# Performance work log

Measured on AMD Instinct MI355X. Metric: run time of the kernel, lower is better.

The kernel has to match this reference:

```python
import jax, jax.numpy as jnp
import numpy as np

C = 32          # in_channels
K = 16          # cluster_nums
G = 16          # grid size per axis (64 / window 4)
FW = 4          # window size
H = G * FW      # 64
NG = G ** 3     # 4096 nodes
NC = NG // K    # 256 nodes per cluster (balanced)
EPS = 1e-5


def setup_inputs():
    key = jax.random.key(0)
    ks = jax.random.split(key, 10)
    def w(k, shape, s=0.05):
        return jax.random.normal(k, shape, jnp.float32) * s
    # balanced cluster assignment (each cluster has exactly NC nodes)
    rng = np.random.RandomState(0)
    ci = np.repeat(np.arange(K, dtype=np.int32), NC)
    rng.shuffle(ci)
    return {
        "x_concat": jax.random.normal(ks[0], (1, H, H, H, C), jnp.float32),
        "cluster_index": jnp.asarray(ci),
        # per-cluster Adjacent_matrix params (1x1 conv == per-pixel linear)
        "conv1_w": w(ks[1], (K, 2 * C, C)), "conv1_b": jnp.zeros((K, 2 * C)),
        "bn1_g": jnp.ones((K, 2 * C)), "bn1_b": jnp.zeros((K, 2 * C)),
        "conv2_w": w(ks[2], (K, 3 * C, 2 * C)), "conv2_b": jnp.zeros((K, 3 * C)),
        "bn2_g": jnp.ones((K, 3 * C)), "bn2_b": jnp.zeros((K, 3 * C)),
        "conv3_w": w(ks[3], (K, 3 * C)), "conv3_b": jnp.zeros((K,)),
        # per-cluster GCN params
        "gcn_w": w(ks[4], (K, 2 * C, C)),
        "bn3_g": jnp.ones((K, C)), "bn3_b": jnp.zeros((K, C)),
        # shared MLP producing spatial weight [C,C] from centroid
        "mlp_w1": w(ks[5], (C, C * C // 8)), "mlp_b1": jnp.zeros((C * C // 8,)),
        "mlp_w2": w(ks[6], (C * C // 8, C * C // 4)), "mlp_b2": jnp.zeros((C * C // 4,)),
        "mlp_w3": w(ks[7], (C * C // 4, C * C)), "mlp_b3": jnp.zeros((C * C,)),
    }


def _bn(h, g, b, axes):
    # train-mode BatchNorm (biased batch statistics), dropout treated as eval/no-op
    m = h.mean(axes, keepdims=True)
    v = h.var(axes, keepdims=True)
    return (h - m) * jax.lax.rsqrt(v + EPS) * g + b


def _forward(cluster_index, x_concat, conv1_w, conv1_b, bn1_g, bn1_b,
             conv2_w, conv2_b, bn2_g, bn2_b, conv3_w, conv3_b,
             gcn_w, bn3_g, bn3_b,
             mlp_w1, mlp_b1, mlp_w2, mlp_b2, mlp_w3, mlp_b3):
    # window_partition + mean over windows -> [NG, C] node features
    x = x_concat.reshape(1, G, FW, G, FW, G, FW, C).mean(axis=(2, 4, 6)).reshape(NG, C)
    order = jnp.argsort(cluster_index)  # stable: contiguous per-cluster index blocks
    eye = jnp.eye(NC, dtype=x.dtype)
    outs = []
    for i in range(K):  # fixed structural loop over clusters
        idx = order[i * NC:(i + 1) * NC]
        xi = x[idx]                                  # [n, C]
        cent = xi.mean(0)                            # kmeans centroid of cluster
        h = jax.nn.relu(cent @ mlp_w1 + mlp_b1)
        h = jax.nn.relu(h @ mlp_w2 + mlp_b2)
        sw = jax.nn.sigmoid(h @ mlp_w3 + mlp_b3).reshape(C, C)
        # Adjacent_matrix: pairwise |xi - xj| -> 1x1 conv stack -> softmax adjacency
        d = jnp.abs(xi[:, None, :] - xi[None, :, :])  # [n, n, C]
        a = jax.nn.leaky_relu(_bn(jnp.einsum('ijc,oc->ijo', d, conv1_w[i]) + conv1_b[i],
                                  bn1_g[i], bn1_b[i], (0, 1)), 0.2)
        a = jax.nn.leaky_relu(_bn(jnp.einsum('ijc,oc->ijo', a, conv2_w[i]) + conv2_b[i],
                                  bn2_g[i], bn2_b[i], (0, 1)), 0.2)
        logits = jnp.einsum('ijc,c->ij', a, conv3_w[i]) + conv3_b[i]  # symmetric
        adj = jax.nn.softmax(logits - 1e8 * eye, axis=-1)
        # gmul_GCN with edge ops [eye, adj] -> concat([x, adj @ x])
        agg = jnp.concatenate([xi, adj @ xi], axis=-1)  # [n, 2C]
        hi = jax.nn.leaky_relu(agg @ (gcn_w[i] @ sw), 0.2)
        hi = _bn(hi, bn3_g[i], bn3_b[i], (0,))          # BatchNorm1d over nodes
        outs.append(hi)
    # scatter_restore
    x_new = jnp.zeros((NG, C), x.dtype).at[order].set(jnp.concatenate(outs, 0))
    # back to grid, pad (1,2) per spatial dim, unfold 4-windows stride 1
    xg = x_new.reshape(1, G, G, G, C).transpose(0, 4, 1, 2, 3)  # [1,C,G,G,G]
    xp = jnp.pad(xg, ((0, 0), (0, 0), (1, 2), (1, 2), (1, 2)))
    iw = jnp.arange(G)[:, None] + jnp.arange(FW)[None, :]       # [G, FW]
    t = xp[:, :, iw]          # [1,C,G,FW,Gp,Gp]
    t = t[:, :, :, :, iw]     # [1,C,G,FW,G,FW,Gp]
    t = t[..., iw]            # [1,C,G,FW,G,FW,G,FW]
    out = t.transpose(0, 2, 3, 4, 5, 6, 7, 1).reshape(1, H, H, H, C)
    return out + x_concat


def reference(x_concat, cluster_index, conv1_w, conv1_b, bn1_g, bn1_b,
              conv2_w, conv2_b, bn2_g, bn2_b, conv3_w, conv3_b,
              gcn_w, bn3_g, bn3_b,
              mlp_w1, mlp_b1, mlp_w2, mlp_b2, mlp_w3, mlp_b3):
    return _forward(cluster_index, x_concat, conv1_w, conv1_b, bn1_g, bn1_b,
                    conv2_w, conv2_b, bn2_g, bn2_b, conv3_w, conv3_b,
                    gcn_w, bn3_g, bn3_b,
                    mlp_w1, mlp_b1, mlp_w2, mlp_b2, mlp_w3, mlp_b3)
```

## Files before the change

### kernel.cpp

```cpp
#include <hip/hip_runtime.h>
#include <hip/hip_bf16.h>


typedef short bfrag8 __attribute__((ext_vector_type(8)));
typedef float f32x4  __attribute__((ext_vector_type(4)));
typedef int   i32x4  __attribute__((ext_vector_type(4)));
typedef short s4v    __attribute__((ext_vector_type(4)));

#define DI __device__ __forceinline__

DI unsigned short f2bf(float f) {
  return __builtin_bit_cast(unsigned short, __float2bfloat16(f));
}
DI float bf2f(unsigned short u) {
  return __builtin_bit_cast(float, ((unsigned)u) << 16);
}
DI unsigned pack2bf(float lo, float hi) {
  unsigned ulo = __builtin_bit_cast(unsigned, lo) + 0x8000u;
  unsigned uhi = __builtin_bit_cast(unsigned, hi) + 0x8000u;
  return __builtin_amdgcn_perm(uhi, ulo, 0x07060302u);
}
DI bfrag8 scale_frag(bfrag8 v, float sc) {
  i32x4 wi = __builtin_bit_cast(i32x4, v);
  i32x4 o;
#pragma unroll
  for (int j = 0; j < 4; ++j) {
    unsigned u = (unsigned)wi[j];
    float lo = bf2f((unsigned short)(u & 0xffffu));
    float hi = bf2f((unsigned short)(u >> 16));
    o[j] = (int)pack2bf(lo * sc, hi * sc);
  }
  return __builtin_bit_cast(bfrag8, o);
}

__global__ __launch_bounds__(256) void k_prep(
    const float* __restrict__ xc, float* __restrict__ x,
    const float* __restrict__ w1, const float* __restrict__ w2,
    unsigned short* __restrict__ w1b, unsigned short* __restrict__ w2p,
    float* __restrict__ statsz) {
  const int bid = blockIdx.x, tid = threadIdx.x;
  if (bid < 128) {
    int idx = bid * 256 + tid;
    int c4 = idx & 7, g = idx >> 3;
    int gz = g & 15, gy = (g >> 4) & 15, gx = g >> 8;
    f32x4 s = {0.f, 0.f, 0.f, 0.f};
    for (int ix = 0; ix < 4; ++ix)
      for (int iy = 0; iy < 4; ++iy)
        for (int iz = 0; iz < 4; ++iz) {
          int X = gx * 4 + ix, Y = gy * 4 + iy, Z = gz * 4 + iz;
          s += *(const f32x4*)&xc[(size_t)(((X << 6) | Y) << 6 | Z) * 32 + c4 * 4];
        }
    *(f32x4*)&x[(size_t)idx * 4] = s * (1.f / 64.f);
    if (bid < 24) statsz[bid * 256 + tid] = 0.f;
  } else {
    int i = (bid - 128) * 256 + tid;
    if (i < 32768) w1b[i] = f2bf(w1[i]);
    int o = i >> 6, cc = i & 63;
    int s = cc >> 5, kp = cc & 31;
    int src = 32 * s + 16 * ((kp >> 2) & 1) + 4 * (kp >> 3) + (kp & 3);
    w2p[i] = f2bf(w2[(size_t)o * 64 + src]);
  }
}

__global__ __launch_bounds__(256) void k_order(
    const int* __restrict__ ci, const float* __restrict__ x,
    int* __restrict__ order, float* __restrict__ xi,
    unsigned short* __restrict__ xib, float* __restrict__ centb) {
  const int k = blockIdx.x, t = threadIdx.x;
  __shared__ int scnt[256];
  __shared__ int ordl[256];
  __shared__ unsigned short xls[256 * 36];
  __shared__ float red[256];

  int match[16];
  int cnt = 0;
#pragma unroll
  for (int j = 0; j < 16; ++j) { match[j] = (ci[t * 16 + j] == k); cnt += match[j]; }
  scnt[t] = cnt;
  __syncthreads();
  for (int off = 1; off < 256; off <<= 1) {
    int v = (t >= off) ? scnt[t - off] : 0;
    __syncthreads();
    scnt[t] += v;
    __syncthreads();
  }
  int pos = scnt[t] - cnt;
#pragma unroll
  for (int j = 0; j < 16; ++j)
    if (match[j]) ordl[pos++] = t * 16 + j;
  __syncthreads();
  int src = ordl[t];
  order[k * 256 + t] = src;
  const f32x4* xr = (const f32x4*)(x + (size_t)src * 32);
  f32x4* xo = (f32x4*)(xi + ((size_t)k * 256 + t) * 32);
  uint2* xb = (uint2*)(xib + ((size_t)k * 256 + t) * 32);
  uint2* xl = (uint2*)&xls[t * 36];
#pragma unroll
  for (int c = 0; c < 8; ++c) {
    f32x4 v = xr[c];
    xo[c] = v;
    unsigned int lo = f2bf(v[0]) | ((unsigned)f2bf(v[1]) << 16);
    unsigned int hi = f2bf(v[2]) | ((unsigned)f2bf(v[3]) << 16);
    xb[c] = make_uint2(lo, hi);
    xl[c] = make_uint2(lo, hi);
  }
  __syncthreads();

  {
    int c = t & 31, rp = t >> 5;
    float ssum = 0.f;
    for (int r = rp; r < 256; r += 8) ssum += bf2f(xls[r * 36 + c]);
    red[t] = ssum;
  }
  __syncthreads();
  if (t < 32) {
    float tot = 0.f;
#pragma unroll
    for (int g = 0; g < 8; ++g) tot += red[g * 32 + t];
    centb[k * 32 + t] = tot * (1.f / 256.f);
  }
}

__global__ __launch_bounds__(256) void k_mlp(
    const float* __restrict__ centb,
    const float* __restrict__ mw1, const float* __restrict__ mb1,
    const float* __restrict__ mw2, const float* __restrict__ mb2,
    const float* __restrict__ mw3, const float* __restrict__ mb3,
    float* __restrict__ swb) {
  const int k = blockIdx.y, bx = blockIdx.x, t = threadIdx.x;
  __shared__ float cent[32];
  __shared__ float h1[128];
  __shared__ float h2s[256];
  __shared__ float red[256];
  if (t < 32) cent[t] = centb[k * 32 + t];
  __syncthreads();
  if (t < 128) {
    float s = mb1[t];
#pragma unroll
    for (int c = 0; c < 32; ++c) s += cent[c] * mw1[c * 128 + t];
    h1[t] = fmaxf(s, 0.f);
  }
  __syncthreads();
  {
    float s = mb2[t];
    for (int j = 0; j < 128; ++j) s += h1[j] * mw2[j * 256 + t];
    h2s[t] = fmaxf(s, 0.f);
  }
  __syncthreads();
  const int o = bx * 64 + (t & 63);
  const int part = t >> 6;
  float s = 0.f;
  const float* m3 = mw3 + (size_t)(part * 64) * 1024 + o;
#pragma unroll 8
  for (int j = 0; j < 64; ++j) s += h2s[part * 64 + j] * m3[j * 1024];
  red[t] = s;
  __syncthreads();
  if (t < 64) {
    float tot = red[t] + red[t + 64] + red[t + 128] + red[t + 192] + mb3[o];
    swb[k * 1024 + o] = 1.f / (1.f + __expf(-tot));
  }
}

template <int MODE>
__global__ __launch_bounds__(256, (MODE == 1) ? 3 : 4) void k_conv(
    const float* __restrict__ xi,
    const unsigned short* __restrict__ w1b,
    const unsigned short* __restrict__ w2p,
    float* stats1, float* stats2,
    const float* __restrict__ bn1g, const float* __restrict__ bn1b,
    const float* __restrict__ bn2g, const float* __restrict__ bn2b,
    const float* __restrict__ c3w,
    float* __restrict__ logits) {
  const int k   = blockIdx.y;
  const int t36 = (MODE == 2) ? (blockIdx.x >> 2) : blockIdx.x;
  int a = 0, rem = t36;
  while (rem >= 8 - a) { rem -= 8 - a; ++a; }
  const int b = a + rem;
  const float w = (a == b) ? 1.f : 2.f;

  const int tid = threadIdx.x;
  const int lane = tid & 63;
  const int wv  = tid >> 6;
  const int l15 = lane & 15;
  const int lg  = lane >> 4;

  int Pb0, Qb;
  if constexpr (MODE == 2) {
    const int sub = blockIdx.x & 3;
    Pb0 = a * 32 + (sub >> 1) * 16;
    Qb  = b * 32 + (sub & 1) * 16;
  } else {
    Pb0 = a * 32;
    Qb  = b * 32;
  }

  constexpr int NF  = (MODE == 0) ? 4 : 6;
  constexpr int NCH = NF * 4;
  constexpr int QGN = (MODE == 2) ? 1 : 2;
  constexpr int XPR = (MODE == 2) ? 16 : 32;

  __shared__ __align__(16) float xp[XPR][32];
  __shared__ float sred[(MODE <= 1) ? 192 : 1];
  __shared__ __align__(16) float s1s[(MODE >= 1) ? 64 : 1];
  __shared__ __align__(16) float t1s[(MODE >= 1) ? 64 : 1];
  __shared__ __align__(16) float sw2s[(MODE == 2) ? 96 : 1];
  __shared__ __align__(16) float cb2s[(MODE == 2) ? 96 : 1];
  __shared__ __align__(16) float s42s[(MODE == 2) ? 96 : 1];
  __shared__ float lt[(MODE == 2) ? 16 : 1][17];

  const float* xik = xi + (size_t)k * 8192;

  if constexpr (MODE == 2) {
    if (tid < 128) {
      int r = tid >> 3, c4 = (tid & 7) * 4;
      *(f32x4*)&xp[r][c4] = *(const f32x4*)(xik + (size_t)(Pb0 + r) * 32 + c4);
    }
  } else {
    int r = tid >> 3, c4 = (tid & 7) * 4;
    *(f32x4*)&xp[r][c4] = *(const f32x4*)(xik + (size_t)(Pb0 + r) * 32 + c4);
  }
  if constexpr (MODE <= 1) {
    if (tid < 192) sred[tid] = 0.f;
  }
  if constexpr (MODE >= 1) {
    if (tid < 64) {
      const int ch = tid;
      float sum = stats1[k * 128 + 2 * ch], sqv = stats1[k * 128 + 2 * ch + 1];
      float mean = sum * (1.f / 16384.f);
      float var  = sqv * (1.f / 16384.f) - mean * mean;
      float s = bn1g[k * 64 + ch] * rsqrtf(fmaxf(var, 0.f) + 1e-5f);
      s1s[ch] = s;
      t1s[ch] = bn1b[k * 64 + ch] - mean * s;
    }
  }
  if constexpr (MODE == 2) {
    if (tid >= 64 && tid < 160) {
      const int ch = tid - 64;
      float sum = stats2[k * 192 + 2 * ch], sqv = stats2[k * 192 + 2 * ch + 1];
      float mean = sum * (1.f / 16384.f);
      float var  = sqv * (1.f / 16384.f) - mean * mean;
      float s2 = bn2g[k * 96 + ch] * rsqrtf(fmaxf(var, 0.f) + 1e-5f);
      float t2 = bn2b[k * 96 + ch] - mean * s2;
      float w3 = c3w[k * 96 + ch];
      sw2s[ch] = s2 * w3;
      cb2s[ch] = t2 * w3;
      s42s[ch] = copysignf(0.4f, w3);
    }
  }

  float qv[QGN][8];
#pragma unroll
  for (int qg = 0; qg < QGN; ++qg) {
    const f32x4* src = (const f32x4*)(xik + (size_t)(Qb + qg * 16 + l15) * 32 + lg * 8);
    f32x4 v0 = src[0], v1 = src[1];
#pragma unroll
    for (int j = 0; j < 4; ++j) { qv[qg][j] = v0[j]; qv[qg][4 + j] = v1[j]; }
  }

  bfrag8 B1[4];
  {
    const unsigned short* w1k = w1b + k * 2048;
#pragma unroll
    for (int f = 0; f < 4; ++f)
      B1[f] = *(const bfrag8*)(w1k + (16 * f + l15) * 32 + lg * 8);
  }
  bfrag8 B2[6][2];
  if constexpr (MODE >= 1) {
    const unsigned short* w2k = w2p + k * 6144;
#pragma unroll
    for (int f2 = 0; f2 < 6; ++f2) {
      B2[f2][0] = *(const bfrag8*)(w2k + (16 * f2 + l15) * 64 + lg * 8);
      B2[f2][1] = *(const bfrag8*)(w2k + (16 * f2 + l15) * 64 + 32 + lg * 8);
    }
  }

  float ss[24], sq[24];
#pragma unroll
  for (int i = 0; i < 24; ++i) { ss[i] = 0.f; sq[i] = 0.f; }

  __syncthreads();

  if constexpr (MODE >= 1) {
#pragma unroll
    for (int f = 0; f < 4; ++f)
      B1[f] = scale_frag(B1[f], s1s[16 * f + l15]);
  }
  if constexpr (MODE == 2) {
#pragma unroll
    for (int f2 = 0; f2 < 6; ++f2) {
      float sc = sw2s[16 * f2 + l15];
      B2[f2][0] = scale_frag(B2[f2][0], sc);
      B2[f2][1] = scale_frag(B2[f2][1], sc);
    }
  }

  const f32x4 z = {0.f, 0.f, 0.f, 0.f};

  bfrag8 dfa[(MODE <= 1) ? 4 : 1];
  if constexpr (MODE <= 1) {
#pragma unroll
    for (int rp = 0; rp < 4; ++rp) {
      const int pl = rp >> 1, qg = rp & 1;
      const int plocal = wv * 8 + pl * 4;
      const float* xpp = &xp[plocal][lg * 8];
      f32x4 p0 = *(const f32x4*)xpp;
      f32x4 p1 = *(const f32x4*)(xpp + 4);
      float pvv[8];
#pragma unroll
      for (int j = 0; j < 4; ++j) { pvv[j] = p0[j]; pvv[4 + j] = p1[j]; }
      unsigned dw[4];
#pragma unroll
      for (int wj = 0; wj < 4; ++wj) {
        float d0 = fabsf(qv[qg][2 * wj]     - pvv[2 * wj]);
        float d1 = fabsf(qv[qg][2 * wj + 1] - pvv[2 * wj + 1]);
        dw[wj] = pack2bf(d0, d1);
      }
      i32x4 dwi = {(int)dw[0], (int)dw[1], (int)dw[2], (int)dw[3]};
      dfa[rp] = __builtin_bit_cast(bfrag8, dwi);
    }
  }

#pragma unroll
  for (int rp = 0; rp < 4; ++rp) {
    const int plocal = (MODE == 2) ? (wv * 4 + rp) : (wv * 8 + (rp >> 1) * 4);
    const int pglob  = Pb0 + plocal;

    bfrag8 df;
    if constexpr (MODE == 2) {
      const float* xpp = &xp[plocal][lg * 8];
      f32x4 p0 = *(const f32x4*)xpp;
      f32x4 p1 = *(const f32x4*)(xpp + 4);
      float pvv[8];
#pragma unroll
      for (int j = 0; j < 4; ++j) { pvv[j] = p0[j]; pvv[4 + j] = p1[j]; }
      unsigned dw[4];
#pragma unroll
      for (int wj = 0; wj < 4; ++wj) {
        float d0 = fabsf(qv[0][2 * wj]     - pvv[2 * wj]);
        float d1 = fabsf(qv[0][2 * wj + 1] - pvv[2 * wj + 1]);
        dw[wj] = pack2bf(d0, d1);
      }
      i32x4 dwi = {(int)dw[0], (int)dw[1], (int)dw[2], (int)dw[3]};
      df = __builtin_bit_cast(bfrag8, dwi);
    } else {
      df = dfa[rp];
    }

    f32x4 acc1[4];
    __builtin_amdgcn_s_setprio(1);
#pragma unroll
    for (int f = 0; f < 4; ++f) {
      f32x4 cin;
      if constexpr (MODE == 0) cin = z;
      else cin = *(const f32x4*)&t1s[16 * f + 4 * lg];
      acc1[f] = __builtin_amdgcn_mfma_f32_16x16x32_bf16(B1[f], df, cin, 0, 0, 0);
    }
    __builtin_amdgcn_s_setprio(0);

    if constexpr (MODE == 0) {
#pragma unroll
      for (int f = 0; f < 4; ++f)
#pragma unroll
        for (int r = 0; r < 4; ++r) {
          float h = acc1[f][r];
          ss[f * 4 + r] += h; sq[f * 4 + r] = fmaf(h, h, sq[f * 4 + r]);
        }
    } else {
      unsigned paw[8];
#pragma unroll
      for (int f = 0; f < 4; ++f) {
        float h0 = acc1[f][0], h1 = acc1[f][1], h2 = acc1[f][2], h3 = acc1[f][3];
        h0 = fmaxf(h0, 0.2f * h0); h1 = fmaxf(h1, 0.2f * h1);
        h2 = fmaxf(h2, 0.2f * h2); h3 = fmaxf(h3, 0.2f * h3);
        paw[f * 2]     = pack2bf(h0, h1);
        paw[f * 2 + 1] = pack2bf(h2, h3);
      }
      i32x4 pa0i = {(int)paw[0], (int)paw[1], (int)paw[2], (int)paw[3]};
      i32x4 pa1i = {(int)paw[4], (int)paw[5], (int)paw[6], (int)paw[7]};
      bfrag8 pa0 = __builtin_bit_cast(bfrag8, pa0i);
      bfrag8 pa1 = __builtin_bit_cast(bfrag8, pa1i);

      float lp = 0.f;
      __builtin_amdgcn_s_setprio(1);
#pragma unroll
      for (int f2 = 0; f2 < 6; ++f2) {
        f32x4 cin;
        if constexpr (MODE == 2) cin = *(const f32x4*)&cb2s[16 * f2 + 4 * lg];
        else cin = z;
        f32x4 acc = __builtin_amdgcn_mfma_f32_16x16x32_bf16(B2[f2][0], pa0, cin, 0, 0, 0);
        acc = __builtin_amdgcn_mfma_f32_16x16x32_bf16(B2[f2][1], pa1, acc, 0, 0, 0);
        if constexpr (MODE == 1) {
#pragma unroll
          for (int r = 0; r < 4; ++r) {
            float h = acc[r];
            ss[f2 * 4 + r] += h; sq[f2 * 4 + r] = fmaf(h, h, sq[f2 * 4 + r]);
          }
        } else {
          f32x4 s4 = *(const f32x4*)&s42s[16 * f2 + 4 * lg];
#pragma unroll
          for (int r = 0; r < 4; ++r) {
            float aa = acc[r];
            float ab = fmaxf(aa, -aa);
            lp = fmaf(0.6f, aa, lp);
            lp = fmaf(s4[r], ab, lp);
          }
        }
      }
      __builtin_amdgcn_s_setprio(0);
      if constexpr (MODE == 2) {
        lp += __shfl_xor(lp, 16);
        lp += __shfl_xor(lp, 32);
        if (lg == 0) {
          logits[(size_t)k * 65536 + (size_t)pglob * 256 + Qb + l15] = lp;
          lt[plocal & 15][l15] = lp;
        }
      }
    }
  }

  if constexpr (MODE == 2) {
    if (a != b) {
      __syncthreads();
      const int ql = tid >> 4, pl = tid & 15;
      logits[(size_t)k * 65536 + (size_t)(Qb + ql) * 256 + Pb0 + pl] = lt[pl][ql];
    }
  }

  if constexpr (MODE <= 1) {
#pragma unroll
    for (int i = 0; i < NCH; ++i) {
#pragma unroll
      for (int m = 1; m <= 8; m <<= 1) {
        ss[i] += __shfl_xor(ss[i], m);
        sq[i] += __shfl_xor(sq[i], m);
      }
    }
    if (l15 == 0) {
#pragma unroll
      for (int i = 0; i < NCH; ++i) {
        int ch = 16 * (i >> 2) + 4 * lg + (i & 3);
        atomicAdd(&sred[ch * 2 + 0], ss[i] * w);
        atomicAdd(&sred[ch * 2 + 1], sq[i] * w);
      }
    }
    __syncthreads();
    float* gs = (MODE == 0) ? stats1 : stats2;
    if (tid < 2 * 16 * NF) atomicAdd(&gs[k * (2 * 16 * NF) + tid], sred[tid]);
  }
}

__global__ __launch_bounds__(256) void k_graph(
    const unsigned short* __restrict__ xib,
    const float* __restrict__ logits,
    const float* __restrict__ swb,
    const float* __restrict__ gcnw,
    float* __restrict__ hi,
    float* __restrict__ stats3) {
  const int k  = blockIdx.y;
  const int pc = blockIdx.x;
  const int tid = threadIdx.x;
  __shared__ __align__(16) unsigned char smem[40960];
  unsigned short* xis = (unsigned short*)smem;
  float* wks  = (float*)(smem + 20480);
  float* cbuf = (float*)(smem + 28672);

  {
    const s4v* src = (const s4v*)(xib + (size_t)k * 8192 + tid * 32);
    s4v* dst = (s4v*)&xis[tid * 40];
#pragma unroll
    for (int j = 0; j < 8; ++j) dst[j] = src[j];
  }
  float* swl = cbuf;
  float* gks = cbuf + 1024;
#pragma unroll
  for (int j = 0; j < 4; ++j) swl[tid + j * 256] = swb[k * 1024 + tid + j * 256];
#pragma unroll
  for (int j = 0; j < 8; ++j) gks[tid + j * 256] = gcnw[(size_t)k * 2048 + tid + j * 256];
  __syncthreads();

#pragma unroll
  for (int j = 0; j < 8; ++j) {
    int e = tid + j * 256;
    int u = e >> 5, v = e & 31;
    float s = 0.f;
#pragma unroll
    for (int c = 0; c < 32; ++c) s += gks[u * 32 + c] * swl[c * 32 + v];
    wks[e] = s;
  }
  __syncthreads();

  float* es    = cbuf;
  float* axs   = cbuf + 2080;
  float* inv_s = cbuf + 2352;
  float* s3    = cbuf + 2360;
  if (tid < 64) s3[tid] = 0.f;

  const int row = tid >> 5;
  const int s   = tid & 31;
  const int pglob = pc * 8 + row;
  const float* lrow = logits + (size_t)k * 65536 + (size_t)pglob * 256;

  float m = -1e30f;
  for (int q = s; q < 256; q += 32) {
    float v = lrow[q];
    m = (q == pglob) ? m : fmaxf(m, v);
  }
#pragma unroll
  for (int mm = 1; mm < 32; mm <<= 1) m = fmaxf(m, __shfl_xor(m, mm));
  float sum = 0.f;
  for (int q = s; q < 256; q += 32) {
    float e = (q == pglob) ? 0.f : __expf(lrow[q] - m);
    es[row * 260 + q] = e;
    sum += e;
  }
#pragma unroll
  for (int mm = 1; mm < 32; mm <<= 1) sum += __shfl_xor(sum, mm);
  if (s == 0) inv_s[row] = 1.f / sum;
  __syncthreads();

  float a0 = 0.f;
  for (int q = 0; q < 256; ++q)
    a0 += es[row * 260 + q] * bf2f(xis[q * 40 + s]);
  axs[row * 34 + s] = a0 * inv_s[row];
  __syncthreads();

  float h = 0.f;
  for (int u = 0; u < 32; ++u) {
    float xu = bf2f(xis[pglob * 40 + u]);
    float au = axs[row * 34 + u];
    h += xu * wks[u * 32 + s] + au * wks[(32 + u) * 32 + s];
  }
  float v = fmaxf(h, 0.2f * h);
  hi[(size_t)k * 8192 + (size_t)pglob * 32 + s] = v;
  float vs = v, vq = v * v;
  vs += __shfl_xor(vs, 32);
  vq += __shfl_xor(vq, 32);
  if ((tid & 32) == 0) {
    atomicAdd(&s3[s * 2 + 0], vs);
    atomicAdd(&s3[s * 2 + 1], vq);
  }
  __syncthreads();
  if (tid < 64) atomicAdd(&stats3[k * 64 + tid], s3[tid]);
}

__global__ __launch_bounds__(256) void k_bn3(
    const float* __restrict__ hi, const float* __restrict__ stats3,
    const float* __restrict__ g3, const float* __restrict__ b3,
    const int* __restrict__ order, float* __restrict__ xnew) {
  int idx = blockIdx.x * 256 + threadIdx.x;
  int k = idx >> 13, r = (idx >> 5) & 255, c = idx & 31;
  float sum = stats3[k * 64 + c * 2], sqv = stats3[k * 64 + c * 2 + 1];
  const float invN = 1.f / 256.f;
  float mean = sum * invN;
  float var = sqv * invN - mean * mean;
  float s = g3[k * 32 + c] * rsqrtf(fmaxf(var, 0.f) + 1e-5f);
  float t = b3[k * 32 + c] - mean * s;
  xnew[(size_t)order[k * 256 + r] * 32 + c] = hi[idx] * s + t;
}

__global__ __launch_bounds__(256) void k_final(const float* __restrict__ xc,
                                               const float* __restrict__ xnew,
                                               float* __restrict__ out) {
  int idx = blockIdx.x * 256 + threadIdx.x;
  int c4 = idx & 7, v = idx >> 3;
  int z = v & 63, y = (v >> 6) & 63, x = v >> 12;
  int sx = (x >> 2) + (x & 3) - 1;
  int sy = (y >> 2) + (y & 3) - 1;
  int sz = (z >> 2) + (z & 3) - 1;
  f32x4 add = {0.f, 0.f, 0.f, 0.f};
  if ((unsigned)sx < 16u && (unsigned)sy < 16u && (unsigned)sz < 16u)
    add = *(const f32x4*)&xnew[(size_t)(((sx << 4) + sy) * 16 + sz) * 32 + c4 * 4];
  const f32x4 a = *(const f32x4*)&xc[(size_t)idx * 4];
  *(f32x4*)&out[(size_t)idx * 4] = a + add;
}

extern "C" void kernel_launch(void* const* d_in, const int* in_sizes, int n_in,
                              void* d_out, int out_size, void* d_ws, size_t ws_size,
                              hipStream_t stream) {
  const float* xc   = (const float*)d_in[0];
  const int*   ci   = (const int*)  d_in[1];
  const float* c1w  = (const float*)d_in[2];
  const float* bn1g = (const float*)d_in[4];
  const float* bn1b = (const float*)d_in[5];
  const float* c2w  = (const float*)d_in[6];
  const float* bn2g = (const float*)d_in[8];
  const float* bn2b = (const float*)d_in[9];
  const float* c3w  = (const float*)d_in[10];
  const float* gcnw = (const float*)d_in[12];
  const float* bn3g = (const float*)d_in[13];
  const float* bn3b = (const float*)d_in[14];
  const float* mw1  = (const float*)d_in[15];
  const float* mb1  = (const float*)d_in[16];
  const float* mw2  = (const float*)d_in[17];
  const float* mb2  = (const float*)d_in[18];
  const float* mw3  = (const float*)d_in[19];
  const float* mb3  = (const float*)d_in[20];

  float* wsf = (float*)d_ws;
  float*  x      = wsf + 0;
  float*  xi     = wsf + 131072;
  float*  xnew   = wsf + 262144;
  float*  hi     = wsf + 393216;
  float*  swb    = wsf + 524288;
  float*  stats1 = wsf + 557056;
  float*  stats2 = wsf + 559104;
  float*  stats3 = wsf + 562176;
  float*  centb  = wsf + 563200;
  float*  logits = wsf + 567296;
  unsigned char* wsb = (unsigned char*)d_ws;
  int* order = (int*)(wsb + 6463488);
  unsigned short* w1b = (unsigned short*)(wsb + 6463488 + 16384);
  unsigned short* w2p = (unsigned short*)(wsb + 6463488 + 16384 + 65536);
  unsigned short* xib = (unsigned short*)(wsb + 6463488 + 16384 + 65536 + 196608);

  k_prep <<<512, 256, 0, stream>>>(xc, x, c1w, c2w, w1b, w2p, stats1);
  k_order<<<16, 256, 0, stream>>>(ci, x, order, xi, xib, centb);
  k_mlp  <<<dim3(16, 16), 256, 0, stream>>>(centb, mw1, mb1, mw2, mb2, mw3, mb3, swb);
  k_conv<0><<<dim3(36, 16), 256, 0, stream>>>(xi, w1b, w2p, stats1, stats2,
                                              bn1g, bn1b, bn2g, bn2b, c3w, logits);
  k_conv<1><<<dim3(36, 16), 256, 0, stream>>>(xi, w1b, w2p, stats1, stats2,
                                              bn1g, bn1b, bn2g, bn2b, c3w, logits);
  k_conv<2><<<dim3(144, 16), 256, 0, stream>>>(xi, w1b, w2p, stats1, stats2,
                                               bn1g, bn1b, bn2g, bn2b, c3w, logits);
  k_graph<<<dim3(32, 16), 256, 0, stream>>>(xib, logits, swb, gcnw, hi, stats3);
  k_bn3  <<<512, 256, 0, stream>>>(hi, stats3, bn3g, bn3b, order, xnew);
  k_final<<<8192, 256, 0, stream>>>(xc, xnew, (float*)d_out);
}
```

Measured before the change: 103.5 us.

## Fuse BN3 scatter into final kernel via inverse order; persistent conv2 blocks

```diff
diff --git a/kernel.cpp b/kernel.cpp
--- a/kernel.cpp
+++ b/kernel.cpp
@@ -64,7 +64,7 @@
 
 __global__ __launch_bounds__(256) void k_order(
     const int* __restrict__ ci, const float* __restrict__ x,
-    int* __restrict__ order, float* __restrict__ xi,
+    int* __restrict__ order, int* __restrict__ inv, float* __restrict__ xi,
     unsigned short* __restrict__ xib, float* __restrict__ centb) {
   const int k = blockIdx.x, t = threadIdx.x;
   __shared__ int scnt[256];
@@ -91,6 +91,7 @@
   __syncthreads();
   int src = ordl[t];
   order[k * 256 + t] = src;
+  inv[src] = k * 256 + t;
   const f32x4* xr = (const f32x4*)(x + (size_t)src * 32);
   f32x4* xo = (f32x4*)(xi + ((size_t)k * 256 + t) * 32);
   uint2* xb = (uint2*)(xib + ((size_t)k * 256 + t) * 32);
@@ -162,17 +163,14 @@
 }
 
 template <int MODE>
-__global__ __launch_bounds__(256, (MODE == 1) ? 3 : 4) void k_conv(
+__global__ __launch_bounds__(256, (MODE == 1) ? 3 : 4) void k_conv01(
     const float* __restrict__ xi,
     const unsigned short* __restrict__ w1b,
     const unsigned short* __restrict__ w2p,
     float* stats1, float* stats2,
-    const float* __restrict__ bn1g, const float* __restrict__ bn1b,
-    const float* __restrict__ bn2g, const float* __restrict__ bn2b,
-    const float* __restrict__ c3w,
-    float* __restrict__ logits) {
+    const float* __restrict__ bn1g, const float* __restrict__ bn1b) {
   const int k   = blockIdx.y;
-  const int t36 = (MODE == 2) ? (blockIdx.x >> 2) : blockIdx.x;
+  const int t36 = blockIdx.x;
   int a = 0, rem = t36;
   while (rem >= 8 - a) { rem -= 8 - a; ++a; }
   const int b = a + rem;
@@ -183,48 +181,25 @@
   const int wv  = tid >> 6;
   const int l15 = lane & 15;
   const int lg  = lane >> 4;
-
-  int Pb0, Qb;
-  if constexpr (MODE == 2) {
-    const int sub = blockIdx.x & 3;
-    Pb0 = a * 32 + (sub >> 1) * 16;
-    Qb  = b * 32 + (sub & 1) * 16;
-  } else {
-    Pb0 = a * 32;
-    Qb  = b * 32;
-  }
+  const int Pb0 = a * 32, Qb = b * 32;
 
   constexpr int NF  = (MODE == 0) ? 4 : 6;
   constexpr int NCH = NF * 4;
-  constexpr int QGN = (MODE == 2) ? 1 : 2;
-  constexpr int XPR = (MODE == 2) ? 16 : 32;
-
-  __shared__ __align__(16) float xp[XPR][32];
-  __shared__ float sred[(MODE <= 1) ? 192 : 1];
-  __shared__ __align__(16) float s1s[(MODE >= 1) ? 64 : 1];
-  __shared__ __align__(16) float t1s[(MODE >= 1) ? 64 : 1];
-  __shared__ __align__(16) float sw2s[(MODE == 2) ? 96 : 1];
-  __shared__ __align__(16) float cb2s[(MODE == 2) ? 96 : 1];
-  __shared__ __align__(16) float s42s[(MODE == 2) ? 96 : 1];
-  __shared__ float lt[(MODE == 2) ? 16 : 1][17];
+
+  __shared__ __align__(16) float xp[32][32];
+  __shared__ float sred[192];
+  __shared__ __align__(16) float s1s[(MODE == 1) ? 64 : 1];
+  __shared__ __align__(16) float t1s[(MODE == 1) ? 64 : 1];
 
   const float* xik = xi + (size_t)k * 8192;
-
-  if constexpr (MODE == 2) {
-    if (tid < 128) {
-      int r = tid >> 3, c4 = (tid & 7) * 4;
-      *(f32x4*)&xp[r][c4] = *(const f32x4*)(xik + (size_t)(Pb0 + r) * 32 + c4);
-    }
-  } else {
+  {
     int r = tid >> 3, c4 = (tid & 7) * 4;
     *(f32x4*)&xp[r][c4] = *(const f32x4*)(xik + (size_t)(Pb0 + r) * 32 + c4);
   }
-  if constexpr (MODE <= 1) {
-    if (tid < 192) sred[tid] = 0.f;
-  }
-  if constexpr (MODE >= 1) {
-    if (tid < 64) {
-      const int ch = tid;
+  if (tid < 192) sred[tid] = 0.f;
+  if constexpr (MODE == 1) {
+    if (tid >= 192) {
+      const int ch = tid - 192;
       float sum = stats1[k * 128 + 2 * ch], sqv = stats1[k * 128 + 2 * ch + 1];
       float mean = sum * (1.f / 16384.f);
       float var  = sqv * (1.f / 16384.f) - mean * mean;
@@ -233,24 +208,10 @@
       t1s[ch] = bn1b[k * 64 + ch] - mean * s;
     }
   }
-  if constexpr (MODE == 2) {
-    if (tid >= 64 && tid < 160) {
-      const int ch = tid - 64;
-      float sum = stats2[k * 192 + 2 * ch], sqv = stats2[k * 192 + 2 * ch + 1];
-      float mean = sum * (1.f / 16384.f);
-      float var  = sqv * (1.f / 16384.f) - mean * mean;
-      float s2 = bn2g[k * 96 + ch] * rsqrtf(fmaxf(var, 0.f) + 1e-5f);
-      float t2 = bn2b[k * 96 + ch] - mean * s2;
-      float w3 = c3w[k * 96 + ch];
-      sw2s[ch] = s2 * w3;
-      cb2s[ch] = t2 * w3;
-      s42s[ch] = copysignf(0.4f, w3);
-    }
-  }
-
-  float qv[QGN][8];
-#pragma unroll
-  for (int qg = 0; qg < QGN; ++qg) {
+
+  float qv[2][8];
+#pragma unroll
+  for (int qg = 0; qg < 2; ++qg) {
     const f32x4* src = (const f32x4*)(xik + (size_t)(Qb + qg * 16 + l15) * 32 + lg * 8);
     f32x4 v0 = src[0], v1 = src[1];
 #pragma unroll
@@ -265,7 +226,7 @@
       B1[f] = *(const bfrag8*)(w1k + (16 * f + l15) * 32 + lg * 8);
   }
   bfrag8 B2[6][2];
-  if constexpr (MODE >= 1) {
+  if constexpr (MODE == 1) {
     const unsigned short* w2k = w2p + k * 6144;
 #pragma unroll
     for (int f2 = 0; f2 < 6; ++f2) {
@@ -280,72 +241,38 @@
 
   __syncthreads();
 
-  if constexpr (MODE >= 1) {
+  if constexpr (MODE == 1) {
 #pragma unroll
     for (int f = 0; f < 4; ++f)
       B1[f] = scale_frag(B1[f], s1s[16 * f + l15]);
   }
-  if constexpr (MODE == 2) {
-#pragma unroll
-    for (int f2 = 0; f2 < 6; ++f2) {
-      float sc = sw2s[16 * f2 + l15];
-      B2[f2][0] = scale_frag(B2[f2][0], sc);
-      B2[f2][1] = scale_frag(B2[f2][1], sc);
-    }
-  }
 
   const f32x4 z = {0.f, 0.f, 0.f, 0.f};
 
-  bfrag8 dfa[(MODE <= 1) ? 4 : 1];
-  if constexpr (MODE <= 1) {
-#pragma unroll
-    for (int rp = 0; rp < 4; ++rp) {
-      const int pl = rp >> 1, qg = rp & 1;
-      const int plocal = wv * 8 + pl * 4;
-      const float* xpp = &xp[plocal][lg * 8];
-      f32x4 p0 = *(const f32x4*)xpp;
-      f32x4 p1 = *(const f32x4*)(xpp + 4);
-      float pvv[8];
-#pragma unroll
-      for (int j = 0; j < 4; ++j) { pvv[j] = p0[j]; pvv[4 + j] = p1[j]; }
-      unsigned dw[4];
-#pragma unroll
-      for (int wj = 0; wj < 4; ++wj) {
-        float d0 = fabsf(qv[qg][2 * wj]     - pvv[2 * wj]);
-        float d1 = fabsf(qv[qg][2 * wj + 1] - pvv[2 * wj + 1]);
-        dw[wj] = pack2bf(d0, d1);
-      }
-      i32x4 dwi = {(int)dw[0], (int)dw[1], (int)dw[2], (int)dw[3]};
-      dfa[rp] = __builtin_bit_cast(bfrag8, dwi);
-    }
-  }
-
+  bfrag8 dfa[4];
 #pragma unroll
   for (int rp = 0; rp < 4; ++rp) {
-    const int plocal = (MODE == 2) ? (wv * 4 + rp) : (wv * 8 + (rp >> 1) * 4);
-    const int pglob  = Pb0 + plocal;
-
-    bfrag8 df;
-    if constexpr (MODE == 2) {
-      const float* xpp = &xp[plocal][lg * 8];
-      f32x4 p0 = *(const f32x4*)xpp;
-      f32x4 p1 = *(const f32x4*)(xpp + 4);
-      float pvv[8];
-#pragma unroll
-      for (int j = 0; j < 4; ++j) { pvv[j] = p0[j]; pvv[4 + j] = p1[j]; }
-      unsigned dw[4];
-#pragma unroll
-      for (int wj = 0; wj < 4; ++wj) {
-        float d0 = fabsf(qv[0][2 * wj]     - pvv[2 * wj]);
-        float d1 = fabsf(qv[0][2 * wj + 1] - pvv[2 * wj + 1]);
-        dw[wj] = pack2bf(d0, d1);
-      }
-      i32x4 dwi = {(int)dw[0], (int)dw[1], (int)dw[2], (int)dw[3]};
-      df = __builtin_bit_cast(bfrag8, dwi);
-    } else {
-      df = dfa[rp];
-    }
-
+    const int pl = rp >> 1, qg = rp & 1;
+    const int plocal = wv * 8 + pl * 4;
+    const float* xpp = &xp[plocal][lg * 8];
+    f32x4 p0 = *(const f32x4*)xpp;
+    f32x4 p1 = *(const f32x4*)(xpp + 4);
+    float pvv[8];
+#pragma unroll
+    for (int j = 0; j < 4; ++j) { pvv[j] = p0[j]; pvv[4 + j] = p1[j]; }
+    unsigned dw[4];
+#pragma unroll
+    for (int wj = 0; wj < 4; ++wj) {
+      float d0 = fabsf(qv[qg][2 * wj]     - pvv[2 * wj]);
+      float d1 = fabsf(qv[qg][2 * wj + 1] - pvv[2 * wj + 1]);
+      dw[wj] = pack2bf(d0, d1);
+    }
+    i32x4 dwi = {(int)dw[0], (int)dw[1], (int)dw[2], (int)dw[3]};
+    dfa[rp] = __builtin_bit_cast(bfrag8, dwi);
+  }
+
+#pragma unroll
+  for (int rp = 0; rp < 4; ++rp) {
     f32x4 acc1[4];
     __builtin_amdgcn_s_setprio(1);
 #pragma unroll
@@ -353,7 +280,7 @@
       f32x4 cin;
       if constexpr (MODE == 0) cin = z;
       else cin = *(const f32x4*)&t1s[16 * f + 4 * lg];
-      acc1[f] = __builtin_amdgcn_mfma_f32_16x16x32_bf16(B1[f], df, cin, 0, 0, 0);
+      acc1[f] = __builtin_amdgcn_mfma_f32_16x16x32_bf16(B1[f], dfa[rp], cin, 0, 0, 0);
     }
     __builtin_amdgcn_s_setprio(0);
 
@@ -380,72 +307,214 @@
       bfrag8 pa0 = __builtin_bit_cast(bfrag8, pa0i);
       bfrag8 pa1 = __builtin_bit_cast(bfrag8, pa1i);
 
-      float lp = 0.f;
       __builtin_amdgcn_s_setprio(1);
 #pragma unroll
       for (int f2 = 0; f2 < 6; ++f2) {
-        f32x4 cin;
-        if constexpr (MODE == 2) cin = *(const f32x4*)&cb2s[16 * f2 + 4 * lg];
-        else cin = z;
-        f32x4 acc = __builtin_amdgcn_mfma_f32_16x16x32_bf16(B2[f2][0], pa0, cin, 0, 0, 0);
+        f32x4 acc = __builtin_amdgcn_mfma_f32_16x16x32_bf16(B2[f2][0], pa0, z, 0, 0, 0);
         acc = __builtin_amdgcn_mfma_f32_16x16x32_bf16(B2[f2][1], pa1, acc, 0, 0, 0);
-        if constexpr (MODE == 1) {
-#pragma unroll
-          for (int r = 0; r < 4; ++r) {
-            float h = acc[r];
-            ss[f2 * 4 + r] += h; sq[f2 * 4 + r] = fmaf(h, h, sq[f2 * 4 + r]);
-          }
-        } else {
-          f32x4 s4 = *(const f32x4*)&s42s[16 * f2 + 4 * lg];
-#pragma unroll
-          for (int r = 0; r < 4; ++r) {
-            float aa = acc[r];
-            float ab = fmaxf(aa, -aa);
-            lp = fmaf(0.6f, aa, lp);
-            lp = fmaf(s4[r], ab, lp);
-          }
+#pragma unroll
+        for (int r = 0; r < 4; ++r) {
+          float h = acc[r];
+          ss[f2 * 4 + r] += h; sq[f2 * 4 + r] = fmaf(h, h, sq[f2 * 4 + r]);
         }
       }
       __builtin_amdgcn_s_setprio(0);
-      if constexpr (MODE == 2) {
-        lp += __shfl_xor(lp, 16);
-        lp += __shfl_xor(lp, 32);
-        if (lg == 0) {
-          logits[(size_t)k * 65536 + (size_t)pglob * 256 + Qb + l15] = lp;
-          lt[plocal & 15][l15] = lp;
+    }
+  }
+
+#pragma unroll
+  for (int i = 0; i < NCH; ++i) {
+#pragma unroll
+    for (int m = 1; m <= 8; m <<= 1) {
+      ss[i] += __shfl_xor(ss[i], m);
+      sq[i] += __shfl_xor(sq[i], m);
+    }
+  }
+  if (l15 == 0) {
+#pragma unroll
+    for (int i = 0; i < NCH; ++i) {
+      int ch = 16 * (i >> 2) + 4 * lg + (i & 3);
+      atomicAdd(&sred[ch * 2 + 0], ss[i] * w);
+      atomicAdd(&sred[ch * 2 + 1], sq[i] * w);
+    }
+  }
+  __syncthreads();
+  float* gs = (MODE == 0) ? stats1 : stats2;
+  if (tid < 2 * 16 * NF) atomicAdd(&gs[k * (2 * 16 * NF) + tid], sred[tid]);
+}
+
+__global__ __launch_bounds__(256, 4) void k_conv2(
+    const float* __restrict__ xi,
+    const unsigned short* __restrict__ w1b,
+    const unsigned short* __restrict__ w2p,
+    const float* __restrict__ stats1, const float* __restrict__ stats2,
+    const float* __restrict__ bn1g, const float* __restrict__ bn1b,
+    const float* __restrict__ bn2g, const float* __restrict__ bn2b,
+    const float* __restrict__ c3w,
+    float* __restrict__ logits) {
+  const int k  = blockIdx.y;
+  const int bx = blockIdx.x;
+  const int tid = threadIdx.x;
+  const int lane = tid & 63;
+  const int wv  = tid >> 6;
+  const int l15 = lane & 15;
+  const int lg  = lane >> 4;
+
+  __shared__ __align__(16) float xp[16][32];
+  __shared__ __align__(16) float s1s[64];
+  __shared__ __align__(16) float t1s[64];
+  __shared__ __align__(16) float sw2s[96];
+  __shared__ __align__(16) float cb2s[96];
+  __shared__ __align__(16) float s42s[96];
+  __shared__ float lt[16][17];
+
+  const float* xik = xi + (size_t)k * 8192;
+
+  if (tid < 64) {
+    const int ch = tid;
+    float sum = stats1[k * 128 + 2 * ch], sqv = stats1[k * 128 + 2 * ch + 1];
+    float mean = sum * (1.f / 16384.f);
+    float var  = sqv * (1.f / 16384.f) - mean * mean;
+    float s = bn1g[k * 64 + ch] * rsqrtf(fmaxf(var, 0.f) + 1e-5f);
+    s1s[ch] = s;
+    t1s[ch] = bn1b[k * 64 + ch] - mean * s;
+  } else if (tid < 160) {
+    const int ch = tid - 64;
+    float sum = stats2[k * 192 + 2 * ch], sqv = stats2[k * 192 + 2 * ch + 1];
+    float mean = sum * (1.f / 16384.f);
+    float var  = sqv * (1.f / 16384.f) - mean * mean;
+    float s2 = bn2g[k * 96 + ch] * rsqrtf(fmaxf(var, 0.f) + 1e-5f);
+    float t2 = bn2b[k * 96 + ch] - mean * s2;
+    float w3 = c3w[k * 96 + ch];
+    sw2s[ch] = s2 * w3;
+    cb2s[ch] = t2 * w3;
+    s42s[ch] = copysignf(0.4f, w3);
+  }
+
+  bfrag8 B1[4];
+  {
+    const unsigned short* w1k = w1b + k * 2048;
+#pragma unroll
+    for (int f = 0; f < 4; ++f)
+      B1[f] = *(const bfrag8*)(w1k + (16 * f + l15) * 32 + lg * 8);
+  }
+  bfrag8 B2[6][2];
+  {
+    const unsigned short* w2k = w2p + k * 6144;
+#pragma unroll
+    for (int f2 = 0; f2 < 6; ++f2) {
+      B2[f2][0] = *(const bfrag8*)(w2k + (16 * f2 + l15) * 64 + lg * 8);
+      B2[f2][1] = *(const bfrag8*)(w2k + (16 * f2 + l15) * 64 + 32 + lg * 8);
+    }
+  }
+  __syncthreads();
+#pragma unroll
+  for (int f = 0; f < 4; ++f)
+    B1[f] = scale_frag(B1[f], s1s[16 * f + l15]);
+#pragma unroll
+  for (int f2 = 0; f2 < 6; ++f2) {
+    float sc = sw2s[16 * f2 + l15];
+    B2[f2][0] = scale_frag(B2[f2][0], sc);
+    B2[f2][1] = scale_frag(B2[f2][1], sc);
+  }
+
+  for (int st = bx; st < 144; st += 64) {
+    const int t36 = st >> 2, sub = st & 3;
+    int a = 0, rem = t36;
+    while (rem >= 8 - a) { rem -= 8 - a; ++a; }
+    const int b = a + rem;
+    const int Pb0 = a * 32 + (sub >> 1) * 16;
+    const int Qb  = b * 32 + (sub & 1) * 16;
+
+    __syncthreads();
+    if (tid < 128) {
+      int r = tid >> 3, c4 = (tid & 7) * 4;
+      *(f32x4*)&xp[r][c4] = *(const f32x4*)(xik + (size_t)(Pb0 + r) * 32 + c4);
+    }
+    __syncthreads();
+
+    float qv8[8];
+    {
+      const f32x4* src = (const f32x4*)(xik + (size_t)(Qb + l15) * 32 + lg * 8);
+      f32x4 v0 = src[0], v1 = src[1];
+#pragma unroll
+      for (int j = 0; j < 4; ++j) { qv8[j] = v0[j]; qv8[4 + j] = v1[j]; }
+    }
+
+#pragma unroll
+    for (int rp = 0; rp < 4; ++rp) {
+      const int plocal = wv * 4 + rp;
+      const int pglob  = Pb0 + plocal;
+
+      const float* xpp = &xp[plocal][lg * 8];
+      f32x4 p0 = *(const f32x4*)xpp;
+      f32x4 p1 = *(const f32x4*)(xpp + 4);
+      float pvv[8];
+#pragma unroll
+      for (int j = 0; j < 4; ++j) { pvv[j] = p0[j]; pvv[4 + j] = p1[j]; }
+      unsigned dw[4];
+#pragma unroll
+      for (int wj = 0; wj < 4; ++wj) {
+        float d0 = fabsf(qv8[2 * wj]     - pvv[2 * wj]);
+        float d1 = fabsf(qv8[2 * wj + 1] - pvv[2 * wj + 1]);
+        dw[wj] = pack2bf(d0, d1);
+      }
+      i32x4 dwi = {(int)dw[0], (int)dw[1], (int)dw[2], (int)dw[3]};
+      bfrag8 df = __builtin_bit_cast(bfrag8, dwi);
+
+      f32x4 acc1[4];
+      __builtin_amdgcn_s_setprio(1);
+#pragma unroll
+      for (int f = 0; f < 4; ++f) {
+        f32x4 cin = *(const f32x4*)&t1s[16 * f + 4 * lg];
+        acc1[f] = __builtin_amdgcn_mfma_f32_16x16x32_bf16(B1[f], df, cin, 0, 0, 0);
+      }
+      __builtin_amdgcn_s_setprio(0);
+
+      unsigned paw[8];
+#pragma unroll
+      for (int f = 0; f < 4; ++f) {
+        float h0 = acc1[f][0], h1 = acc1[f][1], h2 = acc1[f][2], h3 = acc1[f][3];
+        h0 = fmaxf(h0, 0.2f * h0); h1 = fmaxf(h1, 0.2f * h1);
+        h2 = fmaxf(h2, 0.2f * h2); h3 = fmaxf(h3, 0.2f * h3);
+        paw[f * 2]     = pack2bf(h0, h1);
+        paw[f * 2 + 1] = pack2bf(h2, h3);
+      }
+      i32x4 pa0i = {(int)paw[0], (int)paw[1], (int)paw[2], (int)paw[3]};
+      i32x4 pa1i = {(int)paw[4], (int)paw[5], (int)paw[6], (int)paw[7]};
+      bfrag8 pa0 = __builtin_bit_cast(bfrag8, pa0i);
+      bfrag8 pa1 = __builtin_bit_cast(bfrag8, pa1i);
+
+      float lp = 0.f;
+      __builtin_amdgcn_s_setprio(1);
+#pragma unroll
+      for (int f2 = 0; f2 < 6; ++f2) {
+        f32x4 cin = *(const f32x4*)&cb2s[16 * f2 + 4 * lg];
+        f32x4 acc = __builtin_amdgcn_mfma_f32_16x16x32_bf16(B2[f2][0], pa0, cin, 0, 0, 0);
+        acc = __builtin_amdgcn_mfma_f32_16x16x32_bf16(B2[f2][1], pa1, acc, 0, 0, 0);
+        f32x4 s4 = *(const f32x4*)&s42s[16 * f2 + 4 * lg];
+#pragma unroll
+        for (int r = 0; r < 4; ++r) {
+          float aa = acc[r];
+          float ab = fmaxf(aa, -aa);
+          lp = fmaf(0.6f, aa, lp);
+          lp = fmaf(s4[r], ab, lp);
         }
       }
-    }
-  }
-
-  if constexpr (MODE == 2) {
+      __builtin_amdgcn_s_setprio(0);
+      lp += __shfl_xor(lp, 16);
+      lp += __shfl_xor(lp, 32);
+      if (lg == 0) {
+        logits[(size_t)k * 65536 + (size_t)pglob * 256 + Qb + l15] = lp;
+        lt[plocal][l15] = lp;
+      }
+    }
+
+    __syncthreads();
     if (a != b) {
-      __syncthreads();
       const int ql = tid >> 4, pl = tid & 15;
       logits[(size_t)k * 65536 + (size_t)(Qb + ql) * 256 + Pb0 + pl] = lt[pl][ql];
     }
-  }
-
-  if constexpr (MODE <= 1) {
-#pragma unroll
-    for (int i = 0; i < NCH; ++i) {
-#pragma unroll
-      for (int m = 1; m <= 8; m <<= 1) {
-        ss[i] += __shfl_xor(ss[i], m);
-        sq[i] += __shfl_xor(sq[i], m);
-      }
-    }
-    if (l15 == 0) {
-#pragma unroll
-      for (int i = 0; i < NCH; ++i) {
-        int ch = 16 * (i >> 2) + 4 * lg + (i & 3);
-        atomicAdd(&sred[ch * 2 + 0], ss[i] * w);
-        atomicAdd(&sred[ch * 2 + 1], sq[i] * w);
-      }
-    }
-    __syncthreads();
-    float* gs = (MODE == 0) ? stats1 : stats2;
-    if (tid < 2 * 16 * NF) atomicAdd(&gs[k * (2 * 16 * NF) + tid], sred[tid]);
   }
 }
 
@@ -543,33 +612,42 @@
   if (tid < 64) atomicAdd(&stats3[k * 64 + tid], s3[tid]);
 }
 
-__global__ __launch_bounds__(256) void k_bn3(
-    const float* __restrict__ hi, const float* __restrict__ stats3,
+__global__ __launch_bounds__(256) void k_final(
+    const float* __restrict__ xc, const float* __restrict__ hi,
+    const float* __restrict__ stats3,
     const float* __restrict__ g3, const float* __restrict__ b3,
-    const int* __restrict__ order, float* __restrict__ xnew) {
-  int idx = blockIdx.x * 256 + threadIdx.x;
-  int k = idx >> 13, r = (idx >> 5) & 255, c = idx & 31;
-  float sum = stats3[k * 64 + c * 2], sqv = stats3[k * 64 + c * 2 + 1];
-  const float invN = 1.f / 256.f;
-  float mean = sum * invN;
-  float var = sqv * invN - mean * mean;
-  float s = g3[k * 32 + c] * rsqrtf(fmaxf(var, 0.f) + 1e-5f);
-  float t = b3[k * 32 + c] - mean * s;
-  xnew[(size_t)order[k * 256 + r] * 32 + c] = hi[idx] * s + t;
-}
-
-__global__ __launch_bounds__(256) void k_final(const float* __restrict__ xc,
-                                               const float* __restrict__ xnew,
-                                               float* __restrict__ out) {
-  int idx = blockIdx.x * 256 + threadIdx.x;
+    const int* __restrict__ inv, float* __restrict__ out) {
+  const int tid = threadIdx.x;
+  __shared__ float cs[512], ct[512];
+#pragma unroll
+  for (int j = 0; j < 2; ++j) {
+    int ch = tid * 2 + j;
+    int kk = ch >> 5, c = ch & 31;
+    float sum = stats3[kk * 64 + c * 2], sqv = stats3[kk * 64 + c * 2 + 1];
+    float mean = sum * (1.f / 256.f);
+    float var = sqv * (1.f / 256.f) - mean * mean;
+    float s = g3[kk * 32 + c] * rsqrtf(fmaxf(var, 0.f) + 1e-5f);
+    cs[ch] = s;
+    ct[ch] = b3[kk * 32 + c] - mean * s;
+  }
+  __syncthreads();
+
+  int idx = blockIdx.x * 256 + tid;
   int c4 = idx & 7, v = idx >> 3;
   int z = v & 63, y = (v >> 6) & 63, x = v >> 12;
   int sx = (x >> 2) + (x & 3) - 1;
   int sy = (y >> 2) + (y & 3) - 1;
   int sz = (z >> 2) + (z & 3) - 1;
   f32x4 add = {0.f, 0.f, 0.f, 0.f};
-  if ((unsigned)sx < 16u && (unsigned)sy < 16u && (unsigned)sz < 16u)
-    add = *(const f32x4*)&xnew[(size_t)(((sx << 4) + sy) * 16 + sz) * 32 + c4 * 4];
+  if ((unsigned)sx < 16u && (unsigned)sy < 16u && (unsigned)sz < 16u) {
+    int fg = ((sx << 4) + sy) * 16 + sz;
+    int pi = inv[fg];
+    int kk = pi >> 8;
+    f32x4 h = *(const f32x4*)&hi[(size_t)pi * 32 + c4 * 4];
+    int cb = kk * 32 + c4 * 4;
+#pragma unroll
+    for (int j = 0; j < 4; ++j) add[j] = h[j] * cs[cb + j] + ct[cb + j];
+  }
   const f32x4 a = *(const f32x4*)&xc[(size_t)idx * 4];
   *(f32x4*)&out[(size_t)idx * 4] = a + add;
 }
@@ -599,7 +677,6 @@
   float* wsf = (float*)d_ws;
   float*  x      = wsf + 0;
   float*  xi     = wsf + 131072;
-  float*  xnew   = wsf + 262144;
   float*  hi     = wsf + 393216;
   float*  swb    = wsf + 524288;
   float*  stats1 = wsf + 557056;
@@ -612,17 +689,15 @@
   unsigned short* w1b = (unsigned short*)(wsb + 6463488 + 16384);
   unsigned short* w2p = (unsigned short*)(wsb + 6463488 + 16384 + 65536);
   unsigned short* xib = (unsigned short*)(wsb + 6463488 + 16384 + 65536 + 196608);
+  int* inv = (int*)(wsb + 6463488 + 16384 + 65536 + 196608 + 262144);
 
   k_prep <<<512, 256, 0, stream>>>(xc, x, c1w, c2w, w1b, w2p, stats1);
-  k_order<<<16, 256, 0, stream>>>(ci, x, order, xi, xib, centb);
+  k_order<<<16, 256, 0, stream>>>(ci, x, order, inv, xi, xib, centb);
   k_mlp  <<<dim3(16, 16), 256, 0, stream>>>(centb, mw1, mb1, mw2, mb2, mw3, mb3, swb);
-  k_conv<0><<<dim3(36, 16), 256, 0, stream>>>(xi, w1b, w2p, stats1, stats2,
-                                              bn1g, bn1b, bn2g, bn2b, c3w, logits);
-  k_conv<1><<<dim3(36, 16), 256, 0, stream>>>(xi, w1b, w2p, stats1, stats2,
-                                              bn1g, bn1b, bn2g, bn2b, c3w, logits);
-  k_conv<2><<<dim3(144, 16), 256, 0, stream>>>(xi, w1b, w2p, stats1, stats2,
-                                               bn1g, bn1b, bn2g, bn2b, c3w, logits);
+  k_conv01<0><<<dim3(36, 16), 256, 0, stream>>>(xi, w1b, w2p, stats1, stats2, bn1g, bn1b);
+  k_conv01<1><<<dim3(36, 16), 256, 0, stream>>>(xi, w1b, w2p, stats1, stats2, bn1g, bn1b);
+  k_conv2<<<dim3(64, 16), 256, 0, stream>>>(xi, w1b, w2p, stats1, stats2,
+                                            bn1g, bn1b, bn2g, bn2b, c3w, logits);
   k_graph<<<dim3(32, 16), 256, 0, stream>>>(xib, logits, swb, gcnw, hi, stats3);
-  k_bn3  <<<512, 256, 0, stream>>>(hi, stats3, bn3g, bn3b, order, xnew);
-  k_final<<<8192, 256, 0, stream>>>(xc, xnew, (float*)d_out);
-}
+  k_final<<<8192, 256, 0, stream>>>(xc, hi, stats3, bn3g, bn3b, inv, (float*)d_out);
+}
```

New measurement: 104.9 us. Within noise of the previous version (+1.3%).
